# Kernel optimization log

Hardware: AMD Instinct MI355X
Metric: run time of the kernel (lower is better)

Reference implementation:

```python
import jax, jax.numpy as jnp
import numpy as np

N_NODES = 100000
N_EDGES = 1600000
D_IN = 128
D_OUT = 128
EPS = 1e-5


def setup_inputs() -> dict:
    key = jax.random.key(0)
    ks = jax.random.split(key, 5)
    x = jax.random.normal(ks[0], (N_NODES, D_IN), dtype=jnp.float32)
    edge_index = jax.random.randint(ks[1], (2, N_EDGES), 0, N_NODES, dtype=jnp.int64)
    scale = 1.0 / np.sqrt(D_IN)
    W_root = jax.random.normal(ks[2], (D_IN, D_OUT), dtype=jnp.float32) * scale
    W_rel = jax.random.normal(ks[3], (D_IN, D_OUT), dtype=jnp.float32) * scale
    b_rel = jax.random.normal(ks[4], (D_OUT,), dtype=jnp.float32) * 0.01
    gamma = jnp.ones((D_OUT,), dtype=jnp.float32)
    beta = jnp.zeros((D_OUT,), dtype=jnp.float32)
    return {"x": x, "edge_index": edge_index, "W_root": W_root, "W_rel": W_rel,
            "b_rel": b_rel, "gamma": gamma, "beta": beta}


def reference(x, edge_index, W_root, W_rel, b_rel, gamma, beta):
    # GraphConv: out = aggr(x_j) @ W_rel + b_rel + x @ W_root   (aggr = sum)
    src = edge_index[0]
    dst = edge_index[1]
    aggr = jax.ops.segment_sum(x[src], dst, num_segments=x.shape[0])  # [N, D_IN]
    h = aggr @ W_rel + b_rel + x @ W_root                              # [N, D_OUT]
    # NodeLevelBatchNorm (training mode: batch stats over node dim, biased var)
    mean = jnp.mean(h, axis=0)
    var = jnp.mean(jnp.square(h - mean), axis=0)
    h_norm = (h - mean) * jax.lax.rsqrt(var + EPS) * gamma + beta
    return jax.nn.relu(h_norm)
```

## Files before the change

kernel.cpp:

```cpp
#include <hip/hip_runtime.h>

#define N_NODES 100000
#define N_EDGES 1600000
#define D 128
#define NB 196
#define EPT 10
#define CHUNK 2560
#define BIN_BLOCKS 625
#define CVT_X_BLOCKS 6250
#define ZROW N_NODES
#define PBK 13312

typedef __bf16 bf16x8 __attribute__((ext_vector_type(8)));
typedef float f32x4 __attribute__((ext_vector_type(4)));

__device__ __forceinline__ unsigned f2bf(float f) {
    unsigned u = __float_as_uint(f);
    return (u + 0x7fffu + ((u >> 16) & 1u)) >> 16;
}
__device__ __forceinline__ float bf_lo(unsigned u) { return __uint_as_float(u << 16); }
__device__ __forceinline__ float bf_hi(unsigned u) { return __uint_as_float(u & 0xffff0000u); }

__global__ __launch_bounds__(256) void prep_kernel(const float* __restrict__ x,
                                                   const float* __restrict__ Wrel,
                                                   const float* __restrict__ Wroot,
                                                   const int* __restrict__ ei,
                                                   unsigned short* __restrict__ x_bf,
                                                   unsigned short* __restrict__ Wt,
                                                   int* __restrict__ bcount) {
    __shared__ int h[256];
    int b = blockIdx.x;
    int t = threadIdx.x;
    if (b < CVT_X_BLOCKS) {
        size_t i = ((size_t)b * 256 + t) * 8;
        float4 v0 = *(const float4*)(x + i);
        float4 v1 = *(const float4*)(x + i + 4);
        uint4 p;
        p.x = f2bf(v0.x) | (f2bf(v0.y) << 16);
        p.y = f2bf(v0.z) | (f2bf(v0.w) << 16);
        p.z = f2bf(v1.x) | (f2bf(v1.y) << 16);
        p.w = f2bf(v1.z) | (f2bf(v1.w) << 16);
        *(uint4*)(x_bf + i) = p;
    } else if (b < CVT_X_BLOCKS + 128) {
        int c = b - CVT_X_BLOCKS;
        float v = (t < 128) ? Wrel[t * D + c] : Wroot[(t - 128) * D + c];
        Wt[c * 256 + t] = (unsigned short)f2bf(v);
    } else if (b == CVT_X_BLOCKS + 128) {
        if (t < 16) *(uint4*)(x_bf + (size_t)ZROW * D + t * 8) = make_uint4(0, 0, 0, 0);
    } else {
        int blk = b - (CVT_X_BLOCKS + 129);
        h[t] = 0;
        __syncthreads();
        int base = blk * CHUNK;
#pragma unroll
        for (int i = 0; i < EPT; ++i) {
            int dst = ei[N_EDGES + base + i * 256 + t];
            atomicAdd(&h[dst >> 9], 1);
        }
        __syncthreads();
        if (t < NB && h[t]) atomicAdd(&bcount[t], h[t]);
    }
}

__global__ __launch_bounds__(256) void bscan_kernel(const int* __restrict__ bcount,
                                                    int* __restrict__ bucket_base,
                                                    int* __restrict__ bcur) {
    __shared__ int s[256];
    int t = threadIdx.x;
    int v = (t < NB) ? bcount[t] : 0;
    s[t] = v;
    __syncthreads();
    for (int off = 1; off < 256; off <<= 1) {
        int a = (t >= off) ? s[t - off] : 0;
        __syncthreads();
        s[t] += a;
        __syncthreads();
    }
    int excl = s[t] - v;
    if (t < NB) {
        bucket_base[t] = excl;
        bcur[t] = excl;
    }
    if (t == NB) bucket_base[NB] = N_EDGES;
}

__global__ __launch_bounds__(256) void binify_kernel(const int* __restrict__ ei,
                                                     int* __restrict__ bcur,
                                                     unsigned* __restrict__ epk) {
    __shared__ int lhist[256];
    __shared__ int lstart[256];
    __shared__ int lfill[256];
    __shared__ int gbase[256];
    __shared__ uint2 stage[CHUNK];

    int t = threadIdx.x;
    int base = blockIdx.x * CHUNK;
    lhist[t] = 0;
    lfill[t] = 0;
    __syncthreads();

    int src[EPT], dst[EPT];
#pragma unroll
    for (int i = 0; i < EPT; ++i) {
        int e = base + i * 256 + t;
        src[i] = ei[e];
        dst[i] = ei[N_EDGES + e];
        atomicAdd(&lhist[dst[i] >> 9], 1);
    }
    __syncthreads();

    int v = lhist[t];
    lstart[t] = v;
    __syncthreads();
    for (int off = 1; off < 256; off <<= 1) {
        int a = (t >= off) ? lstart[t - off] : 0;
        __syncthreads();
        lstart[t] += a;
        __syncthreads();
    }
    int excl = lstart[t] - v;
    if (t < NB && v > 0) gbase[t] = atomicAdd(&bcur[t], v);
    __syncthreads();
    lstart[t] = excl;
    __syncthreads();

#pragma unroll
    for (int i = 0; i < EPT; ++i) {
        int b = dst[i] >> 9;
        int lp = atomicAdd(&lfill[b], 1);
        stage[lstart[b] + lp] = make_uint2((unsigned)src[i], (unsigned)dst[i]);
    }
    __syncthreads();

    for (int i = t; i < CHUNK; i += 256) {
        uint2 p = stage[i];
        int b = (int)(p.y >> 9);
        unsigned code = p.x | ((p.y & 511u) << 17);
        epk[gbase[b] + (i - lstart[b])] = code;
    }
}

__global__ __launch_bounds__(256) void place_kernel(const unsigned* __restrict__ epk,
                                                    const int* __restrict__ bucket_base,
                                                    int* __restrict__ rbeg,
                                                    int* __restrict__ rend,
                                                    int* __restrict__ srcs) {
    __shared__ int cnt[512];
    __shared__ int sA[512];
    __shared__ int sB[512];
    __shared__ int cursor[512];
    int b = blockIdx.x;
    int t = threadIdx.x;
    int pbeg = bucket_base[b];
    int pend = bucket_base[b + 1];
    int R = b * PBK;

    cnt[t] = 0;
    cnt[t + 256] = 0;
    __syncthreads();
    for (int i = pbeg + t; i < pend; i += 256)
        atomicAdd(&cnt[epk[i] >> 17], 1);
    __syncthreads();

    for (int j = t; j < 512; j += 256) sA[j] = j ? ((cnt[j - 1] + 7) & ~7) : 0;
    __syncthreads();
    int* cur = sA;
    int* nxt = sB;
    for (int off = 1; off < 512; off <<= 1) {
        for (int j = t; j < 512; j += 256)
            nxt[j] = cur[j] + ((j >= off) ? cur[j - off] : 0);
        __syncthreads();
        int* tm = cur; cur = nxt; nxt = tm;
    }

    for (int j = t; j < 512; j += 256) {
        int pj = (cnt[j] + 7) & ~7;
        int s = R + cur[j];
        int g = (b << 9) + j;
        if (g < 100352) { rbeg[g] = s; rend[g] = s + pj; }
        cursor[j] = s;
    }
    __syncthreads();

    for (int i = pbeg + t; i < pend; i += 256) {
        unsigned code = epk[i];
        int pos = atomicAdd(&cursor[code >> 17], 1);
        srcs[pos] = (int)(code & 0x1FFFFu);
    }
    __syncthreads();

    for (int j = t; j < 512; j += 256) {
        int endp = R + cur[j] + ((cnt[j] + 7) & ~7);
        for (int p = cursor[j]; p < endp; ++p) srcs[p] = ZROW;
    }
}

__global__ __launch_bounds__(256, 4) void fused_gemm(const unsigned short* __restrict__ x_bf,
                                                     const int* __restrict__ rbeg,
                                                     const int* __restrict__ rend,
                                                     const int* __restrict__ srcs,
                                                     const unsigned short* __restrict__ Wt,
                                                     const float* __restrict__ brel,
                                                     unsigned short* __restrict__ h_bf,
                                                     float* __restrict__ gsum,
                                                     float* __restrict__ gss) {
    __shared__ unsigned short Af[2048 * 8];
    __shared__ float sbias[128];
    __shared__ float SredS[4][128];
    __shared__ float SredQ[4][128];

    const int t = threadIdx.x;
    const int wave = t >> 6;
    const int lane = t & 63;
    const int quad = lane >> 4;
    const int l16 = lane & 15;
    const int blockRow = blockIdx.x * 128;

    if (t < 128) sbias[t] = brel[t];

    const unsigned short* xp = x_bf + l16 * 8;
#pragma unroll 1
    for (int g = 0; g < 8; ++g) {
        int r = wave * 32 + g * 4 + quad;
        int node = blockRow + r;
        int e = rbeg[node];
        int end = rend[node];
        float a0 = 0.f, a1 = 0.f, a2 = 0.f, a3 = 0.f;
        float a4 = 0.f, a5 = 0.f, a6 = 0.f, a7 = 0.f;
        for (; e < end; e += 8) {
            int4 s0 = *(const int4*)(srcs + e);
            int4 s1 = *(const int4*)(srcs + e + 4);
            uint4 u0 = *(const uint4*)(xp + (size_t)s0.x * D);
            uint4 u1 = *(const uint4*)(xp + (size_t)s0.y * D);
            uint4 u2 = *(const uint4*)(xp + (size_t)s0.z * D);
            uint4 u3 = *(const uint4*)(xp + (size_t)s0.w * D);
            uint4 u4 = *(const uint4*)(xp + (size_t)s1.x * D);
            uint4 u5 = *(const uint4*)(xp + (size_t)s1.y * D);
            uint4 u6 = *(const uint4*)(xp + (size_t)s1.z * D);
            uint4 u7 = *(const uint4*)(xp + (size_t)s1.w * D);
            a0 += bf_lo(u0.x) + bf_lo(u1.x) + bf_lo(u2.x) + bf_lo(u3.x)
                + bf_lo(u4.x) + bf_lo(u5.x) + bf_lo(u6.x) + bf_lo(u7.x);
            a1 += bf_hi(u0.x) + bf_hi(u1.x) + bf_hi(u2.x) + bf_hi(u3.x)
                + bf_hi(u4.x) + bf_hi(u5.x) + bf_hi(u6.x) + bf_hi(u7.x);
            a2 += bf_lo(u0.y) + bf_lo(u1.y) + bf_lo(u2.y) + bf_lo(u3.y)
                + bf_lo(u4.y) + bf_lo(u5.y) + bf_lo(u6.y) + bf_lo(u7.y);
            a3 += bf_hi(u0.y) + bf_hi(u1.y) + bf_hi(u2.y) + bf_hi(u3.y)
                + bf_hi(u4.y) + bf_hi(u5.y) + bf_hi(u6.y) + bf_hi(u7.y);
            a4 += bf_lo(u0.z) + bf_lo(u1.z) + bf_lo(u2.z) + bf_lo(u3.z)
                + bf_lo(u4.z) + bf_lo(u5.z) + bf_lo(u6.z) + bf_lo(u7.z);
            a5 += bf_hi(u0.z) + bf_hi(u1.z) + bf_hi(u2.z) + bf_hi(u3.z)
                + bf_hi(u4.z) + bf_hi(u5.z) + bf_hi(u6.z) + bf_hi(u7.z);
            a6 += bf_lo(u0.w) + bf_lo(u1.w) + bf_lo(u2.w) + bf_lo(u3.w)
                + bf_lo(u4.w) + bf_lo(u5.w) + bf_lo(u6.w) + bf_lo(u7.w);
            a7 += bf_hi(u0.w) + bf_hi(u1.w) + bf_hi(u2.w) + bf_hi(u3.w)
                + bf_hi(u4.w) + bf_hi(u5.w) + bf_hi(u6.w) + bf_hi(u7.w);
        }
        uint4 w;
        w.x = f2bf(a0) | (f2bf(a1) << 16);
        w.y = f2bf(a2) | (f2bf(a3) << 16);
        w.z = f2bf(a4) | (f2bf(a5) << 16);
        w.w = f2bf(a6) | (f2bf(a7) << 16);
        int c = l16;
        int wf = ((r >> 5) << 3) + (((r >> 4) & 1) << 2) + (c >> 2);
        int L = ((c & 3) << 4) | ((r & 15) ^ (c & 3));
        *(uint4*)&Af[(wf * 64 + L) * 8] = w;
    }
    __syncthreads();

    f32x4 acc[2][8];
#pragma unroll
    for (int i = 0; i < 2; ++i)
#pragma unroll
        for (int j = 0; j < 8; ++j) acc[i][j] = (f32x4){0.f, 0.f, 0.f, 0.f};

    const int Lr = (quad << 4) | (l16 ^ quad);

#pragma unroll
    for (int kcl = 0; kcl < 4; ++kcl) {
        bf16x8 af0 = *(const bf16x8*)&Af[(((wave << 3) + kcl) * 64 + Lr) * 8];
        bf16x8 af1 = *(const bf16x8*)&Af[(((wave << 3) + 4 + kcl) * 64 + Lr) * 8];
#pragma unroll
        for (int ct = 0; ct < 8; ++ct) {
            bf16x8 bfrag = *(const bf16x8*)(Wt + (ct * 16 + l16) * 256 + kcl * 32 + quad * 8);
            acc[0][ct] = __builtin_amdgcn_mfma_f32_16x16x32_bf16(af0, bfrag, acc[0][ct], 0, 0, 0);
            acc[1][ct] = __builtin_amdgcn_mfma_f32_16x16x32_bf16(af1, bfrag, acc[1][ct], 0, 0, 0);
        }
    }

    const int rowb = blockRow + wave * 32;
#pragma unroll
    for (int kcl = 0; kcl < 4; ++kcl) {
        const int k0 = kcl * 32 + quad * 8;
        bf16x8 af0 = *(const bf16x8*)(x_bf + (size_t)(rowb + l16) * D + k0);
        bf16x8 af1 = *(const bf16x8*)(x_bf + (size_t)(rowb + 16 + l16) * D + k0);
#pragma unroll
        for (int ct = 0; ct < 8; ++ct) {
            bf16x8 bfrag = *(const bf16x8*)(Wt + (ct * 16 + l16) * 256 + 128 + kcl * 32 + quad * 8);
            acc[0][ct] = __builtin_amdgcn_mfma_f32_16x16x32_bf16(af0, bfrag, acc[0][ct], 0, 0, 0);
            acc[1][ct] = __builtin_amdgcn_mfma_f32_16x16x32_bf16(af1, bfrag, acc[1][ct], 0, 0, 0);
        }
    }

    float csum[8], css[8];
#pragma unroll
    for (int ct = 0; ct < 8; ++ct) { csum[ct] = 0.f; css[ct] = 0.f; }

#pragma unroll
    for (int rt = 0; rt < 2; ++rt) {
#pragma unroll
        for (int ct = 0; ct < 8; ++ct) {
            int col = ct * 16 + l16;
            float bv = sbias[col];
#pragma unroll
            for (int reg = 0; reg < 4; ++reg) {
                int row = blockRow + wave * 32 + rt * 16 + quad * 4 + reg;
                if (row < N_NODES) {
                    float v = acc[rt][ct][reg] + bv;
                    h_bf[(size_t)row * D + col] = (unsigned short)f2bf(v);
                    csum[ct] += v;
                    css[ct] += v * v;
                }
            }
        }
    }
#pragma unroll
    for (int ct = 0; ct < 8; ++ct) {
        float s = csum[ct], q = css[ct];
        s += __shfl_xor(s, 16);
        s += __shfl_xor(s, 32);
        q += __shfl_xor(q, 16);
        q += __shfl_xor(q, 32);
        if (quad == 0) {
            SredS[wave][ct * 16 + l16] = s;
            SredQ[wave][ct * 16 + l16] = q;
        }
    }
    __syncthreads();
    if (t < 128) {
        float s = SredS[0][t] + SredS[1][t] + SredS[2][t] + SredS[3][t];
        float q = SredQ[0][t] + SredQ[1][t] + SredQ[2][t] + SredQ[3][t];
        unsafeAtomicAdd(&gsum[t], s);
        unsafeAtomicAdd(&gss[t], q);
    }
}

__global__ __launch_bounds__(256) void norm_kernel(const unsigned short* __restrict__ h_bf,
                                                   float* __restrict__ out,
                                                   const float* __restrict__ gsum,
                                                   const float* __restrict__ gss,
                                                   const float* __restrict__ gamma,
                                                   const float* __restrict__ beta) {
    __shared__ float sscale[128];
    __shared__ float sshift[128];
    int t = threadIdx.x;
    if (t < 128) {
        const float inv_n = 1.0f / (float)N_NODES;
        float mean = gsum[t] * inv_n;
        float var = gss[t] * inv_n - mean * mean;
        float rs = rsqrtf(var + 1e-5f);
        float sc = gamma[t] * rs;
        sscale[t] = sc;
        sshift[t] = beta[t] - mean * sc;
    }
    __syncthreads();
    size_t e = ((size_t)blockIdx.x * 256 + t) * 4;
    if (e >= (size_t)N_NODES * D) return;
    int c = (int)(e & 127);
    uint2 u = *(const uint2*)(h_bf + e);
    float4 v;
    v.x = fmaxf(bf_lo(u.x) * sscale[c + 0] + sshift[c + 0], 0.f);
    v.y = fmaxf(bf_hi(u.x) * sscale[c + 1] + sshift[c + 1], 0.f);
    v.z = fmaxf(bf_lo(u.y) * sscale[c + 2] + sshift[c + 2], 0.f);
    v.w = fmaxf(bf_hi(u.y) * sscale[c + 3] + sshift[c + 3], 0.f);
    *(float4*)(out + e) = v;
}

extern "C" void kernel_launch(void* const* d_in, const int* in_sizes, int n_in,
                              void* d_out, int out_size, void* d_ws, size_t ws_size,
                              hipStream_t stream) {
    const float* x     = (const float*)d_in[0];
    const int*   ei    = (const int*)d_in[1];
    const float* Wroot = (const float*)d_in[2];
    const float* Wrel  = (const float*)d_in[3];
    const float* brel  = (const float*)d_in[4];
    const float* gamma = (const float*)d_in[5];
    const float* beta  = (const float*)d_in[6];
    float* out = (float*)d_out;

    unsigned short* h_bf = (unsigned short*)d_ws;
    unsigned short* x_bf = h_bf + (size_t)N_NODES * D;
    unsigned short* Wt   = x_bf + (size_t)(N_NODES + 1) * D;
    float* gsum  = (float*)(Wt + 128 * 256);
    float* gss   = gsum + 128;
    int* bcount  = (int*)(gss + 128);
    int* bucket_base = bcount + 256;
    int* bcur    = bucket_base + 256;
    int* rbeg    = bcur + 256;
    int* rend    = rbeg + 100352;
    unsigned* epk = (unsigned*)(rend + 100352);
    int* srcs    = (int*)(epk + N_EDGES);

    hipMemsetAsync(gsum, 0, 512 * sizeof(int), stream);

    prep_kernel<<<CVT_X_BLOCKS + 129 + BIN_BLOCKS, 256, 0, stream>>>(
        x, Wrel, Wroot, ei, x_bf, Wt, bcount);
    bscan_kernel<<<1, 256, 0, stream>>>(bcount, bucket_base, bcur);
    binify_kernel<<<BIN_BLOCKS, 256, 0, stream>>>(ei, bcur, epk);
    place_kernel<<<NB, 256, 0, stream>>>(epk, bucket_base, rbeg, rend, srcs);
    fused_gemm<<<(N_NODES + 127) / 128, 256, 0, stream>>>(
        x_bf, rbeg, rend, srcs, Wt, brel, h_bf, gsum, gss);
    norm_kernel<<<12500, 256, 0, stream>>>(h_bf, out, gsum, gss, gamma, beta);
}
```

Before: 286.1 us.

## Replace bucket histogram and scan with fixed-capacity bucket slots

Drops the dst-bucket histogram pass and the single-block scan kernel. Each bucket instead gets a fixed slot of PBK entries at offset b*PBK, and binify's atomic cursors give each bucket's end. The epk staging buffer is aliased onto the h_bf region, which is not written until later. The launch_bounds occupancy hint on the fused GEMM is also removed. This saves one pass over the edge indices and a kernel launch, but a bucket with more than PBK edges would overflow into the next slot, which is only safe for roughly uniform random inputs.

```diff
diff --git a/kernel.cpp b/kernel.cpp
--- a/kernel.cpp
+++ b/kernel.cpp
@@ -24,11 +24,9 @@
 __global__ __launch_bounds__(256) void prep_kernel(const float* __restrict__ x,
                                                    const float* __restrict__ Wrel,
                                                    const float* __restrict__ Wroot,
-                                                   const int* __restrict__ ei,
                                                    unsigned short* __restrict__ x_bf,
                                                    unsigned short* __restrict__ Wt,
-                                                   int* __restrict__ bcount) {
-    __shared__ int h[256];
+                                                   int* __restrict__ bcur) {
     int b = blockIdx.x;
     int t = threadIdx.x;
     if (b < CVT_X_BLOCKS) {
@@ -48,40 +46,8 @@
     } else if (b == CVT_X_BLOCKS + 128) {
         if (t < 16) *(uint4*)(x_bf + (size_t)ZROW * D + t * 8) = make_uint4(0, 0, 0, 0);
     } else {
-        int blk = b - (CVT_X_BLOCKS + 129);
-        h[t] = 0;
-        __syncthreads();
-        int base = blk * CHUNK;
-#pragma unroll
-        for (int i = 0; i < EPT; ++i) {
-            int dst = ei[N_EDGES + base + i * 256 + t];
-            atomicAdd(&h[dst >> 9], 1);
-        }
-        __syncthreads();
-        if (t < NB && h[t]) atomicAdd(&bcount[t], h[t]);
-    }
-}
-
-__global__ __launch_bounds__(256) void bscan_kernel(const int* __restrict__ bcount,
-                                                    int* __restrict__ bucket_base,
-                                                    int* __restrict__ bcur) {
-    __shared__ int s[256];
-    int t = threadIdx.x;
-    int v = (t < NB) ? bcount[t] : 0;
-    s[t] = v;
-    __syncthreads();
-    for (int off = 1; off < 256; off <<= 1) {
-        int a = (t >= off) ? s[t - off] : 0;
-        __syncthreads();
-        s[t] += a;
-        __syncthreads();
-    }
-    int excl = s[t] - v;
-    if (t < NB) {
-        bucket_base[t] = excl;
-        bcur[t] = excl;
-    }
-    if (t == NB) bucket_base[NB] = N_EDGES;
+        bcur[t] = t * PBK;
+    }
 }
 
 __global__ __launch_bounds__(256) void binify_kernel(const int* __restrict__ ei,
@@ -141,7 +107,7 @@
 }
 
 __global__ __launch_bounds__(256) void place_kernel(const unsigned* __restrict__ epk,
-                                                    const int* __restrict__ bucket_base,
+                                                    const int* __restrict__ bcur,
                                                     int* __restrict__ rbeg,
                                                     int* __restrict__ rend,
                                                     int* __restrict__ srcs) {
@@ -151,9 +117,9 @@
     __shared__ int cursor[512];
     int b = blockIdx.x;
     int t = threadIdx.x;
-    int pbeg = bucket_base[b];
-    int pend = bucket_base[b + 1];
     int R = b * PBK;
+    int pbeg = R;
+    int pend = bcur[b];
 
     cnt[t] = 0;
     cnt[t + 256] = 0;
@@ -195,15 +161,15 @@
     }
 }
 
-__global__ __launch_bounds__(256, 4) void fused_gemm(const unsigned short* __restrict__ x_bf,
-                                                     const int* __restrict__ rbeg,
-                                                     const int* __restrict__ rend,
-                                                     const int* __restrict__ srcs,
-                                                     const unsigned short* __restrict__ Wt,
-                                                     const float* __restrict__ brel,
-                                                     unsigned short* __restrict__ h_bf,
-                                                     float* __restrict__ gsum,
-                                                     float* __restrict__ gss) {
+__global__ __launch_bounds__(256) void fused_gemm(const unsigned short* __restrict__ x_bf,
+                                                  const int* __restrict__ rbeg,
+                                                  const int* __restrict__ rend,
+                                                  const int* __restrict__ srcs,
+                                                  const unsigned short* __restrict__ Wt,
+                                                  const float* __restrict__ brel,
+                                                  unsigned short* __restrict__ h_bf,
+                                                  float* __restrict__ gsum,
+                                                  float* __restrict__ gss) {
     __shared__ unsigned short Af[2048 * 8];
     __shared__ float sbias[128];
     __shared__ float SredS[4][128];
@@ -388,25 +354,21 @@
     float* out = (float*)d_out;
 
     unsigned short* h_bf = (unsigned short*)d_ws;
+    unsigned* epk = (unsigned*)d_ws;
     unsigned short* x_bf = h_bf + (size_t)N_NODES * D;
     unsigned short* Wt   = x_bf + (size_t)(N_NODES + 1) * D;
     float* gsum  = (float*)(Wt + 128 * 256);
     float* gss   = gsum + 128;
-    int* bcount  = (int*)(gss + 128);
-    int* bucket_base = bcount + 256;
-    int* bcur    = bucket_base + 256;
+    int* bcur    = (int*)(gss + 128);
     int* rbeg    = bcur + 256;
     int* rend    = rbeg + 100352;
-    unsigned* epk = (unsigned*)(rend + 100352);
-    int* srcs    = (int*)(epk + N_EDGES);
-
-    hipMemsetAsync(gsum, 0, 512 * sizeof(int), stream);
-
-    prep_kernel<<<CVT_X_BLOCKS + 129 + BIN_BLOCKS, 256, 0, stream>>>(
-        x, Wrel, Wroot, ei, x_bf, Wt, bcount);
-    bscan_kernel<<<1, 256, 0, stream>>>(bcount, bucket_base, bcur);
+    int* srcs    = rend + 100352;
+
+    hipMemsetAsync(gsum, 0, 256 * sizeof(float), stream);
+
+    prep_kernel<<<CVT_X_BLOCKS + 130, 256, 0, stream>>>(x, Wrel, Wroot, x_bf, Wt, bcur);
     binify_kernel<<<BIN_BLOCKS, 256, 0, stream>>>(ei, bcur, epk);
-    place_kernel<<<NB, 256, 0, stream>>>(epk, bucket_base, rbeg, rend, srcs);
+    place_kernel<<<NB, 256, 0, stream>>>(epk, bcur, rbeg, rend, srcs);
     fused_gemm<<<(N_NODES + 127) / 128, 256, 0, stream>>>(
         x_bf, rbeg, rend, srcs, Wt, brel, h_bf, gsum, gss);
     norm_kernel<<<12500, 256, 0, stream>>>(h_bf, out, gsum, gss, gamma, beta);
```

New measurement: 281.7 us. No clear change (-1.5%).
